# Kernel optimization log

Measured on AMD Instinct MI355X. Metric: run time of the kernel, lower is better.

## Reference

```python
import jax, jax.numpy as jnp
import numpy as np

# graph sizes
G, P, EP = 128, 256, 1024          # graphs, nodes/graph, edges/graph
N, E = G * P, G * EP
C, KENS, S = 4, 2, 1               # centroids, ensembles, samples
R = S * KENS                       # repeats
F, DE, D, OUT = 64, 16, 128, 10


def setup_inputs() -> dict:
    key = jax.random.key(0)
    ks = jax.random.split(key, 24)
    off = (jnp.arange(G, dtype=jnp.int32) * P)[:, None]
    src = (jax.random.randint(ks[0], (G, EP), 0, P, dtype=jnp.int32) + off).reshape(-1)
    dst = (jax.random.randint(ks[1], (G, EP), 0, P, dtype=jnp.int32) + off).reshape(-1)
    edge_index = jnp.stack([src, dst])            # [2, E], edges stay within graphs
    batch = jnp.repeat(jnp.arange(G, dtype=jnp.int32), P)  # [N]
    rn = lambda k, shp, s: jax.random.normal(k, shp, jnp.float32) * s
    return {
        "x_feat": rn(ks[2], (N, F), 1.0),
        "edge_attr": rn(ks[3], (E, DE), 1.0),
        "W_atom": rn(ks[4], (F, D), 0.1), "b_atom": jnp.zeros((D,), jnp.float32),
        "W_score": rn(ks[5], (D, C * KENS), 0.1),
        "W_edge": rn(ks[6], (DE, D), 0.1),
        "W_b2c": rn(ks[7], (D, D), 0.1),
        "W_bb": rn(ks[8], (D, D), 0.1), "W_bc": rn(ks[9], (D, D), 0.1),
        "W_cb": rn(ks[10], (D, D), 0.1), "W_cc": rn(ks[11], (D, D), 0.1),
        "W_sb": rn(ks[12], (D, D), 0.1), "W_sc": rn(ks[13], (D, D), 0.1),
        "W_inter": rn(ks[14], (D, D), 0.1), "b_inter": jnp.zeros((D,), jnp.float32),
        "W_out": rn(ks[15], (D, OUT), 0.1), "b_out": jnp.zeros((OUT,), jnp.float32),
        "edge_index": edge_index, "batch": batch,
    }


def reference(x_feat, edge_attr, W_atom, b_atom, W_score, W_edge, W_b2c,
              W_bb, W_bc, W_cb, W_cc, W_sb, W_sc, W_inter, b_inter,
              W_out, b_out, edge_index, batch):
    src, dst = edge_index[0], edge_index[1]
    # atom encoder + scorer + softmax sampler (marginals)
    x = x_feat @ W_atom + b_atom                                  # [N,D]
    scores = (x @ W_score).reshape(N, C, KENS)
    marg = jax.nn.softmax(scores, axis=1)                         # over centroids
    nm = jnp.broadcast_to(marg[None], (S, N, C, KENS))            # [S,N,C,KENS]
    nm = jnp.transpose(nm, (0, 3, 2, 1)).reshape(R, C, N)         # [R,C,N]
    em = nm[:, :, src] * nm[:, :, dst]                            # edge_mask [R,C,E]
    # base2centroid: masked MP on base graph + weighted segment-mean pooling
    edge_emb = edge_attr @ W_edge                                 # [E,D]
    h = jax.nn.relu(x @ W_b2c)                                    # [N,D]
    m = h[src] + edge_emb                                         # [E,D]
    agg = jnp.zeros((R, C, N, D), m.dtype).at[:, :, dst].add(em[..., None] * m)
    hm = h[None, None] + agg                                      # [R,C,N,D]
    denom = jnp.zeros((R, C, G), nm.dtype).at[:, :, batch].add(nm)
    num = jnp.zeros((R, C, G, D), hm.dtype).at[:, :, batch].add(nm[..., None] * hm)
    cent_x = jnp.transpose(num / (denom[..., None] + 1e-6), (0, 2, 1, 3))  # [R,G,C,D]
    # intra centroid-pair edge weights: triu pairs + diag, scatter over graphs
    iu, ju = np.triu_indices(C, 1)
    pi = np.concatenate([iu, np.arange(C)])
    pj = np.concatenate([ju, np.arange(C)])
    e2g = batch[src]
    w = jnp.zeros((R, pi.size, G), nm.dtype).at[:, :, e2g].add(
        nm[:, pi][:, :, src] * nm[:, pj][:, :, dst])              # [R,10,G]
    w = w.at[:, -C:, :].multiply(0.5)                             # halve diagonal counts
    wt = jnp.transpose(w, (0, 2, 1))                              # [R,G,10]
    Wcc = jnp.zeros((R, G, C, C), nm.dtype)
    Wcc = Wcc.at[:, :, pi, pj].add(wt).at[:, :, pj, pi].add(wt)   # to_undirected
    dg = jnp.arange(C)
    Wcc = Wcc.at[:, :, dg, dg].multiply(0.5)                      # self loops counted once
    Wcc = Wcc / (jax.lax.stop_gradient(jnp.max(Wcc)) + 1e-9)      # detached-max norm
    # hetero GNN layer: base->base, base->centroid, centroid->centroid, centroid->base
    agg_bb = jnp.zeros((N, D), x.dtype).at[dst].add(x[src] + edge_emb)           # [N,D]
    agg_bc = jnp.transpose(
        jnp.zeros((R, C, G, D), x.dtype).at[:, :, batch].add(nm[..., None] * x[None, None]),
        (0, 2, 1, 3))                                             # [R,G,C,D]
    agg_cc = jnp.einsum('rgij,rgjd->rgid', Wcc, cent_x)
    h_cent = jax.nn.relu(agg_bc @ W_bc + agg_cc @ W_cc + cent_x @ W_sc)          # [R,G,C,D]
    agg_cb = jnp.einsum('rcn,rncd->rnd', nm, h_cent[:, batch])                   # [R,N,D]
    h_base = jax.nn.relu(agg_bb[None] @ W_bb + agg_cb @ W_cb + x[None] @ W_sb)   # [R,N,D]
    # inter-ensemble mean pool, inter head, intra mean graph pool, intra head
    node_emb = jnp.mean(h_base, axis=0) @ W_inter + b_inter                      # [N,D]
    graph_emb = jnp.zeros((G, D), node_emb.dtype).at[batch].add(node_emb) / P    # [G,D]
    return graph_emb @ W_out + b_out                                             # [G,OUT]
```

## Files before the change

kernel.cpp:

```cpp
#include <hip/hip_runtime.h>
#include <hip/hip_bf16.h>

#define Nn 32768
#define Ee 131072
#define Gg 128
#define Dd 128

using bf16 = __hip_bfloat16;
typedef __attribute__((ext_vector_type(8))) short bf16x8;
typedef __attribute__((ext_vector_type(4))) float f32x4;

__device__ __forceinline__ float b2f(bf16 v){ return __bfloat162float(v); }
__device__ __forceinline__ bf16  f2b(float v){ return __float2bfloat16(v); }
__device__ __forceinline__ unsigned short bf16bits(float v){
  union { bf16 b; unsigned short u; } cv; cv.b = f2b(v); return cv.u;
}
__device__ __forceinline__ float bfu(unsigned short u){
  return __uint_as_float((unsigned int)u << 16);
}
__device__ __forceinline__ float upk_x(unsigned int v){ return __uint_as_float(v << 16); }
__device__ __forceinline__ float upk_h(unsigned int v){ return __uint_as_float(v & 0xffff0000u); }

__global__ __launch_bounds__(128)
void k_wrep(const float* __restrict__ Wbb, const float* __restrict__ Wsb,
            const float* __restrict__ Wcb, const float* __restrict__ Wa,
            const float* __restrict__ Wb2c,
            unsigned short* __restrict__ Wbbp, unsigned short* __restrict__ Wsbp,
            unsigned short* __restrict__ Wcbp, unsigned short* __restrict__ Wap,
            unsigned short* __restrict__ Wb2cp) {
  int mat = blockIdx.x >> 7, n = blockIdx.x & 127, k = threadIdx.x;
  if      (mat == 0) Wbbp [n*128 + k] = bf16bits(Wbb [k*128 + n]);
  else if (mat == 1) Wsbp [n*128 + k] = bf16bits(Wsb [k*128 + n]);
  else if (mat == 2) Wcbp [n*128 + k] = bf16bits(Wcb [k*128 + n]);
  else if (mat == 3) { if (k < 64) Wap[n*64 + k] = bf16bits(Wa[k*128 + n]); }
  else               Wb2cp[n*128 + k] = bf16bits(Wb2c[k*128 + n]);
}

__global__ __launch_bounds__(256)
void k_atom(const float* __restrict__ xf, const unsigned short* __restrict__ Wap,
            const float* __restrict__ ba, const float* __restrict__ Wsc,
            const unsigned short* __restrict__ Wb2cp,
            unsigned int* __restrict__ xh, float* __restrict__ nmt) {
  __shared__ unsigned short sxf[64*72];
  __shared__ unsigned short sxb[64*136];
  __shared__ float ss[64*8];
  __shared__ float sWsc[1024];
  int tid = threadIdx.x, n0 = blockIdx.x*64;
  int lane = tid & 63, wv = tid >> 6;
  int m = lane & 15, quad = lane >> 4;
  int rbase = wv*16;
  #pragma unroll
  for (int k = 0; k < 4; ++k) {
    int pos = (tid + k*256)*4;
    int node = pos >> 6, f = pos & 63;
    float4 v = *reinterpret_cast<const float4*>(xf + (size_t)n0*64 + pos);
    ushort4 o;
    o.x = bf16bits(v.x); o.y = bf16bits(v.y); o.z = bf16bits(v.z); o.w = bf16bits(v.w);
    *reinterpret_cast<ushort4*>(&sxf[node*72 + f]) = o;
  }
  for (int j = tid; j < 1024; j += 256) sWsc[j] = Wsc[j];
  __syncthreads();
  f32x4 cx[8];
  #pragma unroll
  for (int nt = 0; nt < 8; ++nt) {
    float bv = ba[nt*16 + m];
    cx[nt] = (f32x4){bv, bv, bv, bv};
  }
  const unsigned short* a1 = &sxf[(rbase + m)*72];
  #pragma unroll
  for (int nt = 0; nt < 8; ++nt) {
    #pragma unroll
    for (int kk = 0; kk < 2; ++kk) {
      int ko = kk*32 + quad*8;
      bf16x8 av = *reinterpret_cast<const bf16x8*>((const short*)a1 + ko);
      bf16x8 bv8 = *reinterpret_cast<const bf16x8*>((const short*)Wap + (nt*16 + m)*64 + ko);
      cx[nt] = __builtin_amdgcn_mfma_f32_16x16x32_bf16(av, bv8, cx[nt], 0, 0, 0);
    }
  }
  #pragma unroll
  for (int nt = 0; nt < 8; ++nt)
    #pragma unroll
    for (int i = 0; i < 4; ++i)
      sxb[(rbase + quad*4 + i)*136 + nt*16 + m] = bf16bits(cx[nt][i]);
  __syncthreads();
  for (int p = tid; p < 512; p += 256) {
    int node = p >> 3, col = p & 7;
    float s = 0.f;
    for (int dd = 0; dd < 128; ++dd)
      s += bfu(sxb[node*136 + dd]) * sWsc[dd*8 + col];
    ss[node*8 + col] = s;
  }
  __syncthreads();
  if (tid < 128) {
    int node = tid >> 1, k = tid & 1;
    float v0 = ss[node*8 + 0 + k], v1 = ss[node*8 + 2 + k];
    float v2 = ss[node*8 + 4 + k], v3 = ss[node*8 + 6 + k];
    float mx = fmaxf(fmaxf(v0, v1), fmaxf(v2, v3));
    float e0 = expf(v0-mx), e1 = expf(v1-mx), e2 = expf(v2-mx), e3 = expf(v3-mx);
    float inv = 1.f / (e0+e1+e2+e3);
    *reinterpret_cast<float4*>(nmt + (size_t)(n0 + node)*8 + k*4) =
        make_float4(e0*inv, e1*inv, e2*inv, e3*inv);
  }
  f32x4 chf[8];
  #pragma unroll
  for (int nt = 0; nt < 8; ++nt) chf[nt] = (f32x4){0.f,0.f,0.f,0.f};
  const unsigned short* a2 = &sxb[(rbase + m)*136];
  #pragma unroll
  for (int nt = 0; nt < 8; ++nt) {
    #pragma unroll
    for (int kk = 0; kk < 4; ++kk) {
      int ko = kk*32 + quad*8;
      bf16x8 av = *reinterpret_cast<const bf16x8*>((const short*)a2 + ko);
      bf16x8 bv8 = *reinterpret_cast<const bf16x8*>((const short*)Wb2cp + (nt*16 + m)*128 + ko);
      chf[nt] = __builtin_amdgcn_mfma_f32_16x16x32_bf16(av, bv8, chf[nt], 0, 0, 0);
    }
  }
  #pragma unroll
  for (int nt = 0; nt < 8; ++nt) {
    #pragma unroll
    for (int i = 0; i < 4; ++i) {
      int row = rbase + quad*4 + i, col = nt*16 + m;
      float hv = fmaxf(chf[nt][i], 0.f);
      unsigned short xb = sxb[row*136 + col];
      xh[(size_t)(n0 + row)*128 + col] =
          ((unsigned int)bf16bits(hv) << 16) | (unsigned int)xb;
    }
  }
}

__global__ __launch_bounds__(256)
void k_gedge(const int* __restrict__ ei, const float* __restrict__ nmt,
             const float* __restrict__ ea,
             int* __restrict__ osrc, int* __restrict__ rowstart,
             float* __restrict__ sea, float* __restrict__ den,
             float* __restrict__ bnmp, float* __restrict__ geap,
             float* __restrict__ wsump) {
  __shared__ __align__(16) char smem[34384];
  int t = threadIdx.x;
  if (blockIdx.x < Gg) {
    int g = blockIdx.x;
    int* cnt    = (int*)smem;
    int* off    = cnt + 256;
    int* sdl    = off + 256;
    int* ssl    = sdl + 1024;
    int* sorder = ssl + 1024;
    float* den8 = (float*)(sorder + 1024);
    cnt[t] = 0;
    if (t < 8) den8[t] = 0.f;
    __syncthreads();
    #pragma unroll
    for (int j = 0; j < 4; ++j) {
      int e = t + j*256;
      int sl = ei[g*1024 + e] - g*256;
      int dl = ei[Ee + g*1024 + e] - g*256;
      ssl[e] = sl; sdl[e] = dl;
      atomicAdd(&cnt[dl], 1);
    }
    {
      const float4* p = reinterpret_cast<const float4*>(nmt + (size_t)(g*256 + t)*8);
      float4 a = p[0], b = p[1];
      float v[8] = {a.x,a.y,a.z,a.w,b.x,b.y,b.z,b.w};
      #pragma unroll
      for (int i = 0; i < 8; ++i) {
        float s = v[i];
        for (int o = 32; o > 0; o >>= 1) s += __shfl_xor(s, o);
        if ((t & 63) == 0) atomicAdd(&den8[i], s);
      }
    }
    __syncthreads();
    off[t] = cnt[t];
    __syncthreads();
    for (int s = 1; s < 256; s <<= 1) {
      int v = (t >= s) ? off[t - s] : 0;
      __syncthreads();
      off[t] += v;
      __syncthreads();
    }
    int startv = off[t] - cnt[t];
    int mycnt = cnt[t];
    rowstart[g*256 + t] = startv;
    off[t] = startv;
    __syncthreads();
    #pragma unroll
    for (int j = 0; j < 4; ++j) {
      int e = t + j*256;
      int pos = atomicAdd(&off[sdl[e]], 1);
      osrc[g*1024 + pos] = g*256 + ssl[e];
      sorder[pos] = e;
    }
    __syncthreads();
    float s0x=0,s0y=0,s0z=0,s0w=0, s1x=0,s1y=0,s1z=0,s1w=0;
    float s2x=0,s2y=0,s2z=0,s2w=0, s3x=0,s3y=0,s3z=0,s3w=0;
    for (int jj = startv; jj < startv + mycnt; ++jj) {
      int e = sorder[jj];
      const float4* er = reinterpret_cast<const float4*>(ea + ((size_t)g*1024 + e)*16);
      float4 a0 = er[0], a1 = er[1], a2 = er[2], a3 = er[3];
      s0x+=a0.x; s0y+=a0.y; s0z+=a0.z; s0w+=a0.w;
      s1x+=a1.x; s1y+=a1.y; s1z+=a1.z; s1w+=a1.w;
      s2x+=a2.x; s2y+=a2.y; s2z+=a2.z; s2w+=a2.w;
      s3x+=a3.x; s3y+=a3.y; s3z+=a3.z; s3w+=a3.w;
    }
    float4* so = reinterpret_cast<float4*>(sea + (size_t)(g*256 + t)*16);
    so[0] = make_float4(s0x,s0y,s0z,s0w);
    so[1] = make_float4(s1x,s1y,s1z,s1w);
    so[2] = make_float4(s2x,s2y,s2z,s2w);
    so[3] = make_float4(s3x,s3y,s3z,s3w);
    if (t < 8) den[t*Gg + g] = den8[t];
  } else {
    int bq = blockIdx.x - Gg;
    float* eaT   = (float*)smem;
    float* salT  = eaT + 16*260;
    float* sbeta = salT + 8*260;
    float* red   = sbeta + 8*260;
    float* sga   = red + 20;
    int g = bq >> 2;
    int ebase = g*1024 + (bq & 3)*256;
    for (int j = t; j < 2080; j += 256) sbeta[j] = 0.f;
    if (t < 20) red[t] = 0.f;
    __syncthreads();
    int sl = ei[ebase + t] - g*256;
    int dl = ei[Ee + ebase + t] - g*256;
    const float4* ps4 = reinterpret_cast<const float4*>(nmt + (size_t)(g*256 + sl)*8);
    const float4* pt4 = reinterpret_cast<const float4*>(nmt + (size_t)(g*256 + dl)*8);
    float4 sv0 = ps4[0], sv1 = ps4[1], tv0 = pt4[0], tv1 = pt4[1];
    float ps[8] = {sv0.x,sv0.y,sv0.z,sv0.w,sv1.x,sv1.y,sv1.z,sv1.w};
    float pt[8] = {tv0.x,tv0.y,tv0.z,tv0.w,tv1.x,tv1.y,tv1.z,tv1.w};
    float w20[20];
    #pragma unroll
    for (int r = 0; r < 2; ++r) {
      int b = r*4;
      w20[r*10+0] = ps[b+0]*pt[b+1]; w20[r*10+1] = ps[b+0]*pt[b+2];
      w20[r*10+2] = ps[b+0]*pt[b+3]; w20[r*10+3] = ps[b+1]*pt[b+2];
      w20[r*10+4] = ps[b+1]*pt[b+3]; w20[r*10+5] = ps[b+2]*pt[b+3];
      w20[r*10+6] = ps[b+0]*pt[b+0]; w20[r*10+7] = ps[b+1]*pt[b+1];
      w20[r*10+8] = ps[b+2]*pt[b+2]; w20[r*10+9] = ps[b+3]*pt[b+3];
    }
    #pragma unroll
    for (int rc = 0; rc < 8; ++rc) {
      float al = ps[rc]*pt[rc]*pt[rc];
      salT[rc*260 + t] = al;
      atomicAdd(&sbeta[rc*260 + sl], al);
    }
    {
      const float4* ea4 = reinterpret_cast<const float4*>(ea + (size_t)ebase*16);
      #pragma unroll
      for (int k = 0; k < 4; ++k) {
        float4 v = ea4[t*4 + k];
        eaT[(k*4+0)*260 + t] = v.x;
        eaT[(k*4+1)*260 + t] = v.y;
        eaT[(k*4+2)*260 + t] = v.z;
        eaT[(k*4+3)*260 + t] = v.w;
      }
    }
    #pragma unroll
    for (int i = 0; i < 20; ++i) {
      for (int o = 32; o > 0; o >>= 1) w20[i] += __shfl_down(w20[i], o);
    }
    if ((t & 63) == 0) {
      #pragma unroll
      for (int i = 0; i < 20; ++i) atomicAdd(&red[i], w20[i]);
    }
    __syncthreads();
    {
      int rc = t >> 5, j = (t >> 1) & 15, hf = t & 1;
      float a = 0.f;
      int eb = hf*128;
      for (int ee = eb; ee < eb + 128; ++ee)
        a += salT[rc*260 + ee] * eaT[j*260 + ee];
      sga[t] = a;
    }
    __syncthreads();
    if ((t & 1) == 0) {
      int rc = t >> 5, j = (t >> 1) & 15;
      geap[(size_t)bq*128 + rc*16 + j] = sga[t] + sga[t+1];
    }
    if (t < 20) wsump[bq*20 + t] = red[t];
    {
      float4* bo = reinterpret_cast<float4*>(bnmp + (size_t)bq*2048 + t*8);
      bo[0] = make_float4(sbeta[0*260+t], sbeta[1*260+t], sbeta[2*260+t], sbeta[3*260+t]);
      bo[1] = make_float4(sbeta[4*260+t], sbeta[5*260+t], sbeta[6*260+t], sbeta[7*260+t]);
    }
  }
}

__global__ __launch_bounds__(128)
void k_wfin(const float* __restrict__ wsump, float* __restrict__ wcc,
            float* __restrict__ maxv) {
  __shared__ float smax[128];
  int t = threadIdx.x;
  float w[20];
  #pragma unroll
  for (int i = 0; i < 20; ++i)
    w[i] = wsump[(t*4+0)*20 + i] + wsump[(t*4+1)*20 + i]
         + wsump[(t*4+2)*20 + i] + wsump[(t*4+3)*20 + i];
  float mx = 0.f;
  #pragma unroll
  for (int r = 0; r < 2; ++r) {
    #pragma unroll
    for (int ij = 0; ij < 16; ++ij) {
      int i = ij >> 2, j = ij & 3;
      float v;
      if (i == j) v = 0.5f * w[r*10 + 6 + i];
      else { int a = i < j ? i : j, b = i < j ? j : i;
             int p = (a == 0) ? (b - 1) : (a == 1) ? (b + 1) : 5;
             v = w[r*10 + p]; }
      wcc[(r*Gg + t)*16 + ij] = v;
      mx = fmaxf(mx, v);
    }
  }
  smax[t] = mx;
  __syncthreads();
  for (int s = 64; s > 0; s >>= 1) {
    if (t < s) smax[t] = fmaxf(smax[t], smax[t + s]);
    __syncthreads();
  }
  if (t == 0) maxv[0] = smax[0];
}

__global__ __launch_bounds__(256)
void k_poolagg(const unsigned int* __restrict__ xh, const float* __restrict__ nmt,
               const float* __restrict__ bnmp, const float* __restrict__ sea,
               const float* __restrict__ We, const int* __restrict__ osrc,
               const int* __restrict__ rowstart,
               unsigned short* __restrict__ aggbb16,
               float* __restrict__ pnum, float* __restrict__ pabc) {
  __shared__ float combN[8*128], combA[8*128];
  int t = threadIdx.x, d = t & 127, q = t >> 7;
  int g = blockIdx.x >> 4, e16 = blockIdx.x & 15;
  int nbase = g*256 + e16*16;
  float w[16];
  #pragma unroll
  for (int j = 0; j < 16; ++j) w[j] = We[j*128 + d];
  float aH[8] = {0,0,0,0,0,0,0,0};
  float aX[8] = {0,0,0,0,0,0,0,0};
  for (int nn = q; nn < 16; nn += 2) {
    int n = nbase + nn;
    int ln = n & 255;
    unsigned int vn = xh[(size_t)n*128 + d];
    float xn = upk_x(vn), hn = upk_h(vn);
    const float4* pp = reinterpret_cast<const float4*>(nmt + (size_t)n*8);
    float4 p0 = pp[0], p1 = pp[1];
    float pc[8] = {p0.x,p0.y,p0.z,p0.w,p1.x,p1.y,p1.z,p1.w};
    float bt[8] = {0,0,0,0,0,0,0,0};
    #pragma unroll
    for (int qq = 0; qq < 4; ++qq) {
      const float4* bp = reinterpret_cast<const float4*>(bnmp + (size_t)(g*4+qq)*2048 + ln*8);
      float4 b0 = bp[0], b1 = bp[1];
      bt[0]+=b0.x; bt[1]+=b0.y; bt[2]+=b0.z; bt[3]+=b0.w;
      bt[4]+=b1.x; bt[5]+=b1.y; bt[6]+=b1.z; bt[7]+=b1.w;
    }
    #pragma unroll
    for (int rc = 0; rc < 8; ++rc) {
      aH[rc] += (pc[rc] + bt[rc])*hn;
      aX[rc] += pc[rc]*xn;
    }
    const float4* sp = reinterpret_cast<const float4*>(sea + (size_t)n*16);
    float4 s0 = sp[0], s1 = sp[1], s2 = sp[2], s3 = sp[3];
    float agg = s0.x*w[0] + s0.y*w[1] + s0.z*w[2] + s0.w*w[3]
              + s1.x*w[4] + s1.y*w[5] + s1.z*w[6] + s1.w*w[7]
              + s2.x*w[8] + s2.y*w[9] + s2.z*w[10]+ s2.w*w[11]
              + s3.x*w[12]+ s3.y*w[13]+ s3.z*w[14]+ s3.w*w[15];
    int start = rowstart[n];
    int end = (ln == 255) ? 1024 : rowstart[n+1];
    for (int jj = start; jj < end; ++jj) {
      int sg = osrc[g*1024 + jj];
      agg += upk_x(xh[(size_t)sg*128 + d]);
    }
    aggbb16[(size_t)n*128 + d] = bf16bits(agg);
  }
  if (q == 1) {
    #pragma unroll
    for (int rc = 0; rc < 8; ++rc) { combN[rc*128+d] = aH[rc]; combA[rc*128+d] = aX[rc]; }
  }
  __syncthreads();
  if (q == 0) {
    #pragma unroll
    for (int rc = 0; rc < 8; ++rc) {
      pnum[(((size_t)rc*Gg + g)*16 + e16)*128 + d] = aH[rc] + combN[rc*128+d];
      pabc[(((size_t)rc*Gg + g)*16 + e16)*128 + d] = aX[rc] + combA[rc*128+d];
    }
  }
}

__global__ __launch_bounds__(128)
void k_hcent(const float* __restrict__ pnum, const float* __restrict__ den,
             const float* __restrict__ pabc, const float* __restrict__ geap,
             const float* __restrict__ We, const float* __restrict__ wcc,
             const float* __restrict__ maxv,
             const float* __restrict__ Wbc, const float* __restrict__ Wcc_,
             const float* __restrict__ Wsc2, float* __restrict__ hcent) {
  __shared__ float scent[512], sbc[512], sccs[512], swcc[16], sgea[64];
  int tid = threadIdx.x, r = blockIdx.x >> 7, g = blockIdx.x & 127;
  float inv = 1.f / (maxv[0] + 1e-9f);
  if (tid < 16) swcc[tid] = wcc[(r*Gg + g)*16 + tid] * inv;
  if (tid < 64) {
    int c = tid >> 4, j = tid & 15;
    int idx = (r*4 + c)*16 + j;
    sgea[tid] = geap[(size_t)(g*4+0)*128 + idx] + geap[(size_t)(g*4+1)*128 + idx]
              + geap[(size_t)(g*4+2)*128 + idx] + geap[(size_t)(g*4+3)*128 + idx];
  }
  __syncthreads();
  for (int c = 0; c < 4; ++c) {
    int rc = r*4 + c;
    float nv = 0.f, av = 0.f;
    #pragma unroll
    for (int s = 0; s < 16; ++s) {
      nv += pnum[(((size_t)rc*Gg + g)*16 + s)*128 + tid];
      av += pabc[(((size_t)rc*Gg + g)*16 + s)*128 + tid];
    }
    #pragma unroll
    for (int j = 0; j < 16; ++j) nv += sgea[c*16 + j] * We[j*128 + tid];
    float dn = den[rc*Gg + g] + 1e-6f;
    scent[c*128 + tid] = nv / dn;
    sbc[c*128 + tid]   = av;
  }
  __syncthreads();
  for (int i = 0; i < 4; ++i) {
    sccs[i*128 + tid] = swcc[i*4+0]*scent[tid]       + swcc[i*4+1]*scent[128 + tid]
                      + swcc[i*4+2]*scent[256 + tid] + swcc[i*4+3]*scent[384 + tid];
  }
  __syncthreads();
  float acc[4] = {0.f, 0.f, 0.f, 0.f};
  for (int k = 0; k < 128; ++k) {
    float wb = Wbc[k*128 + tid], wc = Wcc_[k*128 + tid], ws2 = Wsc2[k*128 + tid];
    #pragma unroll
    for (int c = 0; c < 4; ++c)
      acc[c] += sbc[c*128 + k]*wb + sccs[c*128 + k]*wc + scent[c*128 + k]*ws2;
  }
  #pragma unroll
  for (int c = 0; c < 4; ++c)
    hcent[((r*Gg + g)*4 + c)*128 + tid] = fmaxf(acc[c], 0.f);
}

__global__ __launch_bounds__(256)
void k_hbase(const unsigned short* __restrict__ aggbb16,
             const unsigned int* __restrict__ xh,
             const float* __restrict__ nmt, const float* __restrict__ hcent,
             const unsigned short* __restrict__ Wbbp,
             const unsigned short* __restrict__ Wsbp,
             const unsigned short* __restrict__ Wcbp,
             float* __restrict__ pgsum) {
  __shared__ unsigned short A1[64*136];
  __shared__ unsigned short A2[64*136];
  __shared__ float shc[512];
  __shared__ float snm[256];
  __shared__ float pred[128];
  int tid = threadIdx.x, n0 = blockIdx.x*64, g = n0 >> 8;
  int lane = tid & 63, wv = tid >> 6;
  int m = lane & 15, quad = lane >> 4;
  int rbase = wv*16;
  for (int j = tid; j < 1024; j += 256) {
    int row = j >> 4, col = (j & 15) * 8;
    uint4 v = *reinterpret_cast<const uint4*>(aggbb16 + (size_t)(n0+row)*128 + col);
    *reinterpret_cast<uint4*>(&A1[row*136 + col]) = v;
  }
  for (int j = tid; j < 2048; j += 256) {
    int row = j >> 5, col = (j & 31) * 4;
    uint4 v = *reinterpret_cast<const uint4*>(xh + (size_t)(n0+row)*128 + col);
    uint2 o;
    o.x = (v.x & 0xffffu) | (v.y << 16);
    o.y = (v.z & 0xffffu) | (v.w << 16);
    *reinterpret_cast<uint2*>(&A2[row*136 + col]) = o;
  }
  __syncthreads();
  f32x4 bb[8];
  #pragma unroll
  for (int nt = 0; nt < 8; ++nt) bb[nt] = (f32x4){0.f,0.f,0.f,0.f};
  const short* a1r = (const short*)&A1[(rbase + m)*136];
  const short* a2r = (const short*)&A2[(rbase + m)*136];
  #pragma unroll
  for (int nt = 0; nt < 8; ++nt) {
    #pragma unroll
    for (int kk = 0; kk < 4; ++kk) {
      int ko = kk*32 + quad*8;
      bf16x8 av1 = *reinterpret_cast<const bf16x8*>(a1r + ko);
      bf16x8 wv1 = *reinterpret_cast<const bf16x8*>((const short*)Wbbp + (nt*16 + m)*128 + ko);
      bb[nt] = __builtin_amdgcn_mfma_f32_16x16x32_bf16(av1, wv1, bb[nt], 0, 0, 0);
      bf16x8 av2 = *reinterpret_cast<const bf16x8*>(a2r + ko);
      bf16x8 wv2 = *reinterpret_cast<const bf16x8*>((const short*)Wsbp + (nt*16 + m)*128 + ko);
      bb[nt] = __builtin_amdgcn_mfma_f32_16x16x32_bf16(av2, wv2, bb[nt], 0, 0, 0);
    }
  }
  __syncthreads();
  unsigned short* SB = A2;
  f32x4 msum[8];
  #pragma unroll
  for (int nt = 0; nt < 8; ++nt) msum[nt] = (f32x4){0.f,0.f,0.f,0.f};
  for (int r = 0; r < 2; ++r) {
    for (int j = tid; j < 512; j += 256) shc[j] = hcent[((size_t)(r*Gg + g)*4)*128 + j];
    if (tid < 256) snm[tid] = nmt[(size_t)(n0 + (tid >> 2))*8 + r*4 + (tid & 3)];
    __syncthreads();
    for (int j = tid; j < 8192; j += 256) {
      int node = j >> 7, k = j & 127;
      float v = snm[node*4+0]*shc[k]       + snm[node*4+1]*shc[128 + k]
              + snm[node*4+2]*shc[256 + k] + snm[node*4+3]*shc[384 + k];
      SB[node*136 + k] = bf16bits(v);
    }
    __syncthreads();
    f32x4 aw[8];
    #pragma unroll
    for (int nt = 0; nt < 8; ++nt) aw[nt] = (f32x4){0.f,0.f,0.f,0.f};
    const short* sbr = (const short*)&SB[(rbase + m)*136];
    #pragma unroll
    for (int nt = 0; nt < 8; ++nt) {
      #pragma unroll
      for (int kk = 0; kk < 4; ++kk) {
        int ko = kk*32 + quad*8;
        bf16x8 av = *reinterpret_cast<const bf16x8*>(sbr + ko);
        bf16x8 wvv = *reinterpret_cast<const bf16x8*>((const short*)Wcbp + (nt*16 + m)*128 + ko);
        aw[nt] = __builtin_amdgcn_mfma_f32_16x16x32_bf16(av, wvv, aw[nt], 0, 0, 0);
      }
    }
    #pragma unroll
    for (int nt = 0; nt < 8; ++nt) {
      #pragma unroll
      for (int i = 0; i < 4; ++i)
        msum[nt][i] += 0.5f * fmaxf(bb[nt][i] + aw[nt][i], 0.f);
    }
    __syncthreads();
  }
  if (tid < 128) pred[tid] = 0.f;
  __syncthreads();
  #pragma unroll
  for (int nt = 0; nt < 8; ++nt) {
    float s = msum[nt][0] + msum[nt][1] + msum[nt][2] + msum[nt][3];
    atomicAdd(&pred[nt*16 + m], s);
  }
  __syncthreads();
  if (tid < 128) pgsum[(size_t)blockIdx.x*128 + tid] = pred[tid];
}

__global__ __launch_bounds__(128)
void k_out(const float* __restrict__ pgsum, const float* __restrict__ Wint,
           const float* __restrict__ bint, const float* __restrict__ Wout,
           const float* __restrict__ bout, float* __restrict__ out) {
  __shared__ float ss[128], sge[128];
  int tid = threadIdx.x, g = blockIdx.x;
  float s = pgsum[(size_t)(g*4+0)*128 + tid] + pgsum[(size_t)(g*4+1)*128 + tid]
          + pgsum[(size_t)(g*4+2)*128 + tid] + pgsum[(size_t)(g*4+3)*128 + tid];
  ss[tid] = s * (1.f/256.f);
  __syncthreads();
  float ge = bint[tid];
  for (int k = 0; k < 128; ++k) ge += ss[k] * Wint[k*128 + tid];
  sge[tid] = ge;
  __syncthreads();
  if (tid < 10) {
    float o = bout[tid];
    for (int d = 0; d < 128; ++d) o += sge[d] * Wout[d*10 + tid];
    out[g*10 + tid] = o;
  }
}

extern "C" void kernel_launch(void* const* d_in, const int* in_sizes, int n_in,
                              void* d_out, int out_size, void* d_ws, size_t ws_size,
                              hipStream_t stream) {
  const float* xf   = (const float*)d_in[0];
  const float* ea   = (const float*)d_in[1];
  const float* Wa   = (const float*)d_in[2];
  const float* ba   = (const float*)d_in[3];
  const float* Wsc  = (const float*)d_in[4];
  const float* We   = (const float*)d_in[5];
  const float* Wb2c = (const float*)d_in[6];
  const float* Wbb  = (const float*)d_in[7];
  const float* Wbc  = (const float*)d_in[8];
  const float* Wcb  = (const float*)d_in[9];
  const float* WccW = (const float*)d_in[10];
  const float* Wsb  = (const float*)d_in[11];
  const float* Wsc2 = (const float*)d_in[12];
  const float* Wint = (const float*)d_in[13];
  const float* bint = (const float*)d_in[14];
  const float* Wout = (const float*)d_in[15];
  const float* bout = (const float*)d_in[16];
  const int*   ei   = (const int*)d_in[17];

  float* ws    = (float*)d_ws;
  unsigned int* xh = (unsigned int*)ws;
  float* nmt   = ws + 4194304;
  float* hcent = ws + 4456448;
  float* wcc   = ws + 4587520;
  unsigned short* aggbb16 = (unsigned short*)(ws + 4591616);
  int*   osrc  = (int*)(ws + 6688768);
  int*   rowst = (int*)(ws + 6950912);
  float* sea   = ws + 6983680;
  float* bnmp  = ws + 7507968;
  float* geap  = ws + 8556544;
  float* wsump = ws + 8622080;
  float* pnum  = ws + 8632320;
  float* pabc  = ws + 10729472;
  float* den   = ws + 12826624;
  float* pgsum = ws + 12827648;
  float* maxv  = ws + 12893184;
  unsigned short* Wbbp  = (unsigned short*)(ws + 12893248);
  unsigned short* Wsbp  = (unsigned short*)(ws + 12901440);
  unsigned short* Wcbp  = (unsigned short*)(ws + 12909632);
  unsigned short* Wap   = (unsigned short*)(ws + 12917824);
  unsigned short* Wb2cp = (unsigned short*)(ws + 12921920);

  k_wrep   <<<5*128,   128, 0, stream>>>(Wbb, Wsb, Wcb, Wa, Wb2c,
                                         Wbbp, Wsbp, Wcbp, Wap, Wb2cp);
  k_atom   <<<Nn/64,   256, 0, stream>>>(xf, Wap, ba, Wsc, Wb2cp, xh, nmt);
  k_gedge  <<<Gg+Gg*4, 256, 0, stream>>>(ei, nmt, ea, osrc, rowst, sea, den,
                                         bnmp, geap, wsump);
  k_wfin   <<<1,       128, 0, stream>>>(wsump, wcc, maxv);
  k_poolagg<<<Gg*16,   256, 0, stream>>>(xh, nmt, bnmp, sea, We, osrc, rowst,
                                         aggbb16, pnum, pabc);
  k_hcent  <<<2*Gg,    128, 0, stream>>>(pnum, den, pabc, geap, We, wcc, maxv,
                                         Wbc, WccW, Wsc2, hcent);
  k_hbase  <<<Nn/64,   256, 0, stream>>>(aggbb16, xh, nmt, hcent, Wbbp, Wsbp, Wcbp, pgsum);
  k_out    <<<Gg,      128, 0, stream>>>(pgsum, Wint, bint, Wout, bout, (float*)d_out);
}
```

Baseline: 276.4 us.

## Stage per-graph node features in shared memory for edge gather and pooling

k_poolagg now runs one block per quarter-graph (512 blocks instead of 2048). Each block first loads the whole graph's bf16 x features (64 KB) into LDS, and the neighbour gather reads from LDS instead of scattered global loads. The partial-sum layout changes from 16 to 8 slots per graph, and k_hcent is updated to match. k_gedge also caches the graph's nmt rows in LDS for its per-edge marginal lookups. The cost is fewer, heavier blocks with large LDS use (low occupancy), plus each graph's features being loaded redundantly by four blocks.

```diff
diff --git a/kernel.cpp b/kernel.cpp
--- a/kernel.cpp
+++ b/kernel.cpp
@@ -135,7 +135,7 @@
              float* __restrict__ sea, float* __restrict__ den,
              float* __restrict__ bnmp, float* __restrict__ geap,
              float* __restrict__ wsump) {
-  __shared__ __align__(16) char smem[34384];
+  __shared__ __align__(16) char smem[42576];
   int t = threadIdx.x;
   if (blockIdx.x < Gg) {
     int g = blockIdx.x;
@@ -213,15 +213,17 @@
     float* sbeta = salT + 8*260;
     float* red   = sbeta + 8*260;
     float* sga   = red + 20;
+    float* snmt  = sga + 256;
     int g = bq >> 2;
     int ebase = g*1024 + (bq & 3)*256;
     for (int j = t; j < 2080; j += 256) sbeta[j] = 0.f;
     if (t < 20) red[t] = 0.f;
+    for (int j = t; j < 2048; j += 256) snmt[j] = nmt[(size_t)g*2048 + j];
     __syncthreads();
     int sl = ei[ebase + t] - g*256;
     int dl = ei[Ee + ebase + t] - g*256;
-    const float4* ps4 = reinterpret_cast<const float4*>(nmt + (size_t)(g*256 + sl)*8);
-    const float4* pt4 = reinterpret_cast<const float4*>(nmt + (size_t)(g*256 + dl)*8);
+    const float4* ps4 = reinterpret_cast<const float4*>(snmt + sl*8);
+    const float4* pt4 = reinterpret_cast<const float4*>(snmt + dl*8);
     float4 sv0 = ps4[0], sv1 = ps4[1], tv0 = pt4[0], tv1 = pt4[1];
     float ps[8] = {sv0.x,sv0.y,sv0.z,sv0.w,sv1.x,sv1.y,sv1.z,sv1.w};
     float pt[8] = {tv0.x,tv0.y,tv0.z,tv0.w,tv1.x,tv1.y,tv1.z,tv1.w};
@@ -324,18 +326,20 @@
                const int* __restrict__ rowstart,
                unsigned short* __restrict__ aggbb16,
                float* __restrict__ pnum, float* __restrict__ pabc) {
-  __shared__ float combN[8*128], combA[8*128];
+  __shared__ unsigned short sxg[256*128];
   int t = threadIdx.x, d = t & 127, q = t >> 7;
-  int g = blockIdx.x >> 4, e16 = blockIdx.x & 15;
-  int nbase = g*256 + e16*16;
+  int g = blockIdx.x >> 2, quar = blockIdx.x & 3;
+  for (int j = t; j < 32768; j += 256)
+    sxg[j] = (unsigned short)(xh[(size_t)(g << 8)*128 + j] & 0xffffu);
+  __syncthreads();
   float w[16];
   #pragma unroll
   for (int j = 0; j < 16; ++j) w[j] = We[j*128 + d];
   float aH[8] = {0,0,0,0,0,0,0,0};
   float aX[8] = {0,0,0,0,0,0,0,0};
-  for (int nn = q; nn < 16; nn += 2) {
-    int n = nbase + nn;
-    int ln = n & 255;
+  int nbase = g*256 + quar*64;
+  for (int nn = q; nn < 64; nn += 2) {
+    int n = nbase + nn, ln = n & 255;
     unsigned int vn = xh[(size_t)n*128 + d];
     float xn = upk_x(vn), hn = upk_h(vn);
     const float4* pp = reinterpret_cast<const float4*>(nmt + (size_t)n*8);
@@ -364,21 +368,15 @@
     int end = (ln == 255) ? 1024 : rowstart[n+1];
     for (int jj = start; jj < end; ++jj) {
       int sg = osrc[g*1024 + jj];
-      agg += upk_x(xh[(size_t)sg*128 + d]);
+      agg += bfu(sxg[(sg & 255)*128 + d]);
     }
     aggbb16[(size_t)n*128 + d] = bf16bits(agg);
   }
-  if (q == 1) {
-    #pragma unroll
-    for (int rc = 0; rc < 8; ++rc) { combN[rc*128+d] = aH[rc]; combA[rc*128+d] = aX[rc]; }
-  }
-  __syncthreads();
-  if (q == 0) {
-    #pragma unroll
-    for (int rc = 0; rc < 8; ++rc) {
-      pnum[(((size_t)rc*Gg + g)*16 + e16)*128 + d] = aH[rc] + combN[rc*128+d];
-      pabc[(((size_t)rc*Gg + g)*16 + e16)*128 + d] = aX[rc] + combA[rc*128+d];
-    }
+  int slot = quar*2 + q;
+  #pragma unroll
+  for (int rc = 0; rc < 8; ++rc) {
+    pnum[(((size_t)rc*Gg + g)*8 + slot)*128 + d] = aH[rc];
+    pabc[(((size_t)rc*Gg + g)*8 + slot)*128 + d] = aX[rc];
   }
 }
 
@@ -404,9 +402,9 @@
     int rc = r*4 + c;
     float nv = 0.f, av = 0.f;
     #pragma unroll
-    for (int s = 0; s < 16; ++s) {
-      nv += pnum[(((size_t)rc*Gg + g)*16 + s)*128 + tid];
-      av += pabc[(((size_t)rc*Gg + g)*16 + s)*128 + tid];
+    for (int s = 0; s < 8; ++s) {
+      nv += pnum[(((size_t)rc*Gg + g)*8 + s)*128 + tid];
+      av += pabc[(((size_t)rc*Gg + g)*8 + s)*128 + tid];
     }
     #pragma unroll
     for (int j = 0; j < 16; ++j) nv += sgea[c*16 + j] * We[j*128 + tid];
@@ -602,7 +600,7 @@
   k_gedge  <<<Gg+Gg*4, 256, 0, stream>>>(ei, nmt, ea, osrc, rowst, sea, den,
                                          bnmp, geap, wsump);
   k_wfin   <<<1,       128, 0, stream>>>(wsump, wcc, maxv);
-  k_poolagg<<<Gg*16,   256, 0, stream>>>(xh, nmt, bnmp, sea, We, osrc, rowst,
+  k_poolagg<<<Gg*4,    256, 0, stream>>>(xh, nmt, bnmp, sea, We, osrc, rowst,
                                          aggbb16, pnum, pabc);
   k_hcent  <<<2*Gg,    128, 0, stream>>>(pnum, den, pabc, geap, We, wcc, maxv,
                                          Wbc, WccW, Wsc2, hcent);
```

Result: no change. 276.3 us (-0.0%).
